# Performance work log

Hardware: AMD Instinct MI355X
Metric: run time of the kernel (lower is better)

## Reference

```python
import jax, jax.numpy as jnp
import numpy as np

# Module hyper-parameters (eval mode: remove_rand_on_eval=True => no random additional points)
B, H, C, E = 2, 8, 2048, 1024
D = 64          # head_size
KP = 8          # k (points per query per head)
P = 2 * KP      # num_points = k * 2**rank, rank = 1


def setup_inputs() -> dict:
    key = jax.random.key(0)
    ks = jax.random.split(key, 10)
    x = jax.random.normal(ks[0], (B, C, E), jnp.float32)
    attention_mask = jnp.ones((B, C), jnp.int32)  # accepted but unused, as in the torch forward
    # hyper() outputs (abstract in the class): continuous means in [0, C-1), positive sigmas, values
    means = jax.random.uniform(ks[1], (B, H, C, KP, 1), jnp.float32) * (C - 1)
    sigmas = jax.random.uniform(ks[2], (B, H, C, KP), jnp.float32) * 2.0 + 0.5
    values = jax.random.normal(ks[3], (B, H, C, KP), jnp.float32)
    s_in = 1.0 / np.sqrt(E).astype(np.float32)
    s_u = 1.0 / np.sqrt(H * D).astype(np.float32)
    Wk = jax.random.normal(ks[4], (E, H * D), jnp.float32) * s_in
    Wq = jax.random.normal(ks[5], (E, H * D), jnp.float32) * s_in
    Wv = jax.random.normal(ks[6], (E, H * D), jnp.float32) * s_in
    Wu = jax.random.normal(ks[7], (H * D, E), jnp.float32) * s_u
    bu = jnp.zeros((E,), jnp.float32)
    return dict(x=x, attention_mask=attention_mask, means=means, sigmas=sigmas,
                values=values, Wk=Wk, Wq=Wq, Wv=Wv, Wu=Wu, bu=bu)


def reference(x, attention_mask, means, sigmas, values, Wk, Wq, Wv, Wu, bu):
    b, c, e = x.shape
    h, d, kp, p = H, D, KP, P

    # ---- ngenerate (eval: only the 2**rank = 2 integer corners per mean, clamped in-range) ----
    m = means[..., 0]                                  # (b,h,c,k)
    i0 = jnp.clip(jnp.floor(m).astype(jnp.int32), 0, c - 1)
    i1 = jnp.clip(i0 + 1, 0, c - 1)
    idx = jnp.stack([i0, i1], axis=-1).reshape(b, h, c, p)   # (b,h,c,P)
    idx_fl = idx.astype(jnp.float32)

    # ---- densities: unnormalized Gaussian of each integer point under each of the k means ----
    diff = idx_fl[..., :, None] - m[..., None, :]            # (b,h,c,P,k)
    dens = jnp.exp(-0.5 * (diff / sigmas[..., None, :]) ** 2)

    # ---- nduplicates: zero densities of repeated index tuples (keep first occurrence) ----
    eq = idx[..., :, None] == idx[..., None, :]              # (b,h,c,P,P)
    earlier = jnp.tril(jnp.ones((p, p), bool), k=-1)         # q < p
    dup = jnp.any(eq & earlier, axis=-1)                     # (b,h,c,P)
    dens = jnp.where(dup[..., None], 0.0, dens)

    # normalize over dim=2 (context), exactly as the torch code does
    dens = dens / (dens.sum(axis=2, keepdims=True) + 1e-8)

    # density-weighted continuous values -> per-point weights
    weights = (values[..., None, :] * dens).sum(axis=-1)     # (b,h,c,P)

    # ---- projections ----
    inv_sqrt_d = 1.0 / np.sqrt(d).astype(np.float32)
    Kt = (x @ Wk).reshape(b, c, h, d).transpose(0, 2, 1, 3) * inv_sqrt_d  # (b,h,c,d)
    Qt = (x @ Wq).reshape(b, c, h, d).transpose(0, 2, 1, 3) * inv_sqrt_d
    Vt = (x @ Wv).reshape(b, c, h, d).transpose(0, 2, 1, 3)

    # ---- gather K/V at the sparse indices ----
    flat = idx.reshape(b, h, c * p, 1)
    Kg = jnp.take_along_axis(Kt, flat, axis=2).reshape(b, h, c, p, d)
    Vg = jnp.take_along_axis(Vt, flat, axis=2).reshape(b, h, c, p, d)

    dots = jnp.einsum('bhcd,bhcpd->bhcp', Qt, Kg)
    new_weights = jax.nn.softmax(weights * dots, axis=-1)    # (b,h,c,P)

    head_reps = jnp.einsum('bhcpd,bhcp->bhcd', Vg, new_weights)
    united = head_reps.transpose(0, 2, 1, 3).reshape(b, c, h * d)
    new_out = united @ Wu + bu

    # ---- scatter-add sparse weights into dense attention matrix ----
    bi = jnp.arange(b)[:, None, None, None]
    hi = jnp.arange(h)[None, :, None, None]
    ci = jnp.arange(c)[None, None, :, None]
    attentions = jnp.zeros((b, h, c, c), jnp.float32).at[bi, hi, ci, idx].add(new_weights)

    return new_out, attentions
```

## Files before the change

kernel.cpp:

```cpp
#include <hip/hip_runtime.h>
#include <math.h>
#include <stdint.h>

#define B_ 2
#define H_ 8
#define C_ 2048
#define E_ 1024
#define D_ 64
#define KP_ 8
#define P_ 16
#define HD_ 512
#define ROWS_ 32768
#define M_ 4096

typedef __bf16 bf16x8 __attribute__((ext_vector_type(8)));
typedef float f32x4 __attribute__((ext_vector_type(4)));
typedef uint16_t u16x8 __attribute__((ext_vector_type(8)));

__device__ inline uint16_t f2bf(float f) {
    union { float f; uint32_t u; } v; v.f = f;
    uint32_t u = v.u + 0x7FFF + ((v.u >> 16) & 1);
    return (uint16_t)(u >> 16);
}
__device__ inline float bf2f(uint16_t h) {
    union { uint32_t u; float f; } v; v.u = ((uint32_t)h) << 16;
    return v.f;
}

__device__ inline void gload16(const uint16_t* g, uint16_t* l) {
    __builtin_amdgcn_global_load_lds(
        (const __attribute__((address_space(1))) void*)g,
        (__attribute__((address_space(3))) void*)l, 16, 0, 0);
}

__global__ __launch_bounds__(256) void convert_x_kernel(
    const float* __restrict__ in, uint16_t* __restrict__ out)
{
    const int i = (blockIdx.x * 256 + threadIdx.x) * 8;
    const float4 a = *(const float4*)(in + i);
    const float4 b = *(const float4*)(in + i + 4);
    u16x8 o;
    o[0] = f2bf(a.x); o[1] = f2bf(a.y); o[2] = f2bf(a.z); o[3] = f2bf(a.w);
    o[4] = f2bf(b.x); o[5] = f2bf(b.y); o[6] = f2bf(b.z); o[7] = f2bf(b.w);
    *(u16x8*)(out + i) = o;
}

__global__ __launch_bounds__(256) void convert_wt_kernel(
    const float* __restrict__ Wq, const float* __restrict__ Wk,
    const float* __restrict__ Wv, const float* __restrict__ Wu,
    uint16_t* __restrict__ Wall, uint16_t* __restrict__ Wut)
{
    const int z = blockIdx.z;
    const float* in; uint16_t* out; int R, Cc; float scale;
    if (z == 0)      { in = Wq; out = Wall;                 R = E_;  Cc = HD_; scale = 0.125f; }
    else if (z == 1) { in = Wk; out = Wall + 512 * 1024;    R = E_;  Cc = HD_; scale = 0.125f; }
    else if (z == 2) { in = Wv; out = Wall + 1024 * 1024;   R = E_;  Cc = HD_; scale = 1.0f; }
    else             { in = Wu; out = Wut;                  R = HD_; Cc = E_;  scale = 1.0f; }
    const int tiles_x = Cc >> 5;
    const int tx = blockIdx.x % tiles_x;
    const int ty = blockIdx.x / tiles_x;
    const int r0 = ty * 32, c0 = tx * 32;
    __shared__ float t[32][33];
    const int lx = threadIdx.x & 31, ly = threadIdx.x >> 5;
#pragma unroll
    for (int i = 0; i < 4; ++i)
        t[ly * 4 + i][lx] = in[(size_t)(r0 + ly * 4 + i) * Cc + c0 + lx];
    __syncthreads();
#pragma unroll
    for (int i = 0; i < 4; ++i)
        out[(size_t)(c0 + ly * 4 + i) * R + r0 + lx] = f2bf(t[lx][ly * 4 + i] * scale);
}

__global__ __launch_bounds__(256) void gemm_qkv_kernel(
    const uint16_t* __restrict__ xb, const uint16_t* __restrict__ Wall,
    uint16_t* __restrict__ Qt, uint16_t* __restrict__ Kt,
    uint16_t* __restrict__ Vt)
{
    const int K = E_;
    const int m0 = blockIdx.y * 128;
    const int n0 = blockIdx.x * 128;
    const int z = n0 >> 9;
    uint16_t* __restrict__ Out = (z == 0) ? Qt : (z == 1) ? Kt : Vt;

    __shared__ __align__(16) uint16_t As[128 * 32];
    __shared__ __align__(16) uint16_t Bs[128 * 32];

    const int tid = threadIdx.x;
    const int w = tid >> 6, lane = tid & 63;
    const int wm = w & 1, wn = w >> 1;

    f32x4 acc[4][4] = {};

    const int r0s = (w * 2 + 0) * 16 + (lane >> 2);
    const int r1s = (w * 2 + 1) * 16 + (lane >> 2);
    const int ko  = (lane & 3) * 8;
    const uint16_t* gA0 = xb + (size_t)(m0 + r0s) * K + ko;
    const uint16_t* gA1 = xb + (size_t)(m0 + r1s) * K + ko;
    const uint16_t* gB0 = Wall + (size_t)(n0 + r0s) * K + ko;
    const uint16_t* gB1 = Wall + (size_t)(n0 + r1s) * K + ko;
    uint16_t* lA0 = &As[(w * 2 + 0) * 512];
    uint16_t* lA1 = &As[(w * 2 + 1) * 512];
    uint16_t* lB0 = &Bs[(w * 2 + 0) * 512];
    uint16_t* lB1 = &Bs[(w * 2 + 1) * 512];

    const int fr = lane & 15;
    const int fk = (lane >> 4) * 8;

    for (int k0 = 0; k0 < K; k0 += 32) {
        __syncthreads();
        gload16(gA0 + k0, lA0);
        gload16(gA1 + k0, lA1);
        gload16(gB0 + k0, lB0);
        gload16(gB1 + k0, lB1);
        __syncthreads();
        bf16x8 af[4], bf[4];
#pragma unroll
        for (int t = 0; t < 4; ++t) {
            af[t] = *(const bf16x8*)&As[(wm * 64 + t * 16 + fr) * 32 + fk];
            bf[t] = *(const bf16x8*)&Bs[(wn * 64 + t * 16 + fr) * 32 + fk];
        }
#pragma unroll
        for (int mt = 0; mt < 4; ++mt)
#pragma unroll
            for (int nt = 0; nt < 4; ++nt)
                acc[mt][nt] = __builtin_amdgcn_mfma_f32_16x16x32_bf16(
                    af[mt], bf[nt], acc[mt][nt], 0, 0, 0);
    }

#pragma unroll
    for (int mt = 0; mt < 4; ++mt) {
#pragma unroll
        for (int nt = 0; nt < 4; ++nt) {
            const int nl = (n0 & 511) + wn * 64 + nt * 16 + fr;
            const int h = nl >> 6, d = nl & 63;
#pragma unroll
            for (int r = 0; r < 4; ++r) {
                const int m = m0 + wm * 64 + mt * 16 + (lane >> 4) * 4 + r;
                const int b = m >> 11, c = m & (C_ - 1);
                Out[(((size_t)(b * H_ + h) * C_ + c) << 6) + d] =
                    f2bf(acc[mt][nt][r]);
            }
        }
    }
}

__global__ __launch_bounds__(256) void gemm_out_kernel(
    const uint16_t* __restrict__ U, const uint16_t* __restrict__ Wut,
    const float* __restrict__ bu, float* __restrict__ out)
{
    const int K = HD_;
    const int m0 = blockIdx.y * 128;
    const int n0 = blockIdx.x * 128;

    __shared__ __align__(16) uint16_t As[128 * 32];
    __shared__ __align__(16) uint16_t Bs[128 * 32];

    const int tid = threadIdx.x;
    const int w = tid >> 6, lane = tid & 63;
    const int wm = w & 1, wn = w >> 1;

    f32x4 acc[4][4] = {};

    const int r0s = (w * 2 + 0) * 16 + (lane >> 2);
    const int r1s = (w * 2 + 1) * 16 + (lane >> 2);
    const int ko  = (lane & 3) * 8;
    const uint16_t* gA0 = U + (size_t)(m0 + r0s) * K + ko;
    const uint16_t* gA1 = U + (size_t)(m0 + r1s) * K + ko;
    const uint16_t* gB0 = Wut + (size_t)(n0 + r0s) * K + ko;
    const uint16_t* gB1 = Wut + (size_t)(n0 + r1s) * K + ko;
    uint16_t* lA0 = &As[(w * 2 + 0) * 512];
    uint16_t* lA1 = &As[(w * 2 + 1) * 512];
    uint16_t* lB0 = &Bs[(w * 2 + 0) * 512];
    uint16_t* lB1 = &Bs[(w * 2 + 1) * 512];

    const int fr = lane & 15;
    const int fk = (lane >> 4) * 8;

    for (int k0 = 0; k0 < K; k0 += 32) {
        __syncthreads();
        gload16(gA0 + k0, lA0);
        gload16(gA1 + k0, lA1);
        gload16(gB0 + k0, lB0);
        gload16(gB1 + k0, lB1);
        __syncthreads();
        bf16x8 af[4], bf[4];
#pragma unroll
        for (int t = 0; t < 4; ++t) {
            af[t] = *(const bf16x8*)&As[(wm * 64 + t * 16 + fr) * 32 + fk];
            bf[t] = *(const bf16x8*)&Bs[(wn * 64 + t * 16 + fr) * 32 + fk];
        }
#pragma unroll
        for (int mt = 0; mt < 4; ++mt)
#pragma unroll
            for (int nt = 0; nt < 4; ++nt)
                acc[mt][nt] = __builtin_amdgcn_mfma_f32_16x16x32_bf16(
                    af[mt], bf[nt], acc[mt][nt], 0, 0, 0);
    }

#pragma unroll
    for (int mt = 0; mt < 4; ++mt) {
#pragma unroll
        for (int nt = 0; nt < 4; ++nt) {
            const int n = n0 + wn * 64 + nt * 16 + fr;
            const float bias = bu[n];
#pragma unroll
            for (int r = 0; r < 4; ++r) {
                const int m = m0 + wm * 64 + mt * 16 + (lane >> 4) * 4 + r;
                out[(size_t)m * E_ + n] = acc[mt][nt][r] + bias;
            }
        }
    }
}

__global__ __launch_bounds__(256) void dens_sum_kernel(
    const float* __restrict__ means, const float* __restrict__ sigmas,
    float* __restrict__ S)
{
    const int row = blockIdx.x * 256 + threadIdx.x;
    const int lane = threadIdx.x & 63;
    const int bh = row >> 11;

    const float* mrow = means + (size_t)row * 8;
    const float* srow = sigmas + (size_t)row * 8;
    const float4 ma = *(const float4*)(mrow);
    const float4 mb = *(const float4*)(mrow + 4);
    const float4 sa = *(const float4*)(srow);
    const float4 sb = *(const float4*)(srow + 4);
    const float mm[8] = {ma.x, ma.y, ma.z, ma.w, mb.x, mb.y, mb.z, mb.w};
    const float sg[8] = {sa.x, sa.y, sa.z, sa.w, sb.x, sb.y, sb.z, sb.w};

    int idx[16];
#pragma unroll
    for (int j = 0; j < 8; ++j) {
        int i0 = (int)floorf(mm[j]);
        i0 = min(max(i0, 0), C_ - 1);
        idx[2 * j] = i0;
        idx[2 * j + 1] = min(i0 + 1, C_ - 1);
    }
    unsigned dupm = 0;
#pragma unroll
    for (int p = 1; p < 16; ++p) {
        bool d = false;
#pragma unroll
        for (int q = 0; q < 15; ++q)
            if (q < p) d = d || (idx[q] == idx[p]);
        if (d) dupm |= (1u << p);
    }

#pragma unroll
    for (int p = 0; p < 16; ++p) {
        const float fi = (float)idx[p];
        const bool dup = (dupm >> p) & 1u;
#pragma unroll
        for (int kk = 0; kk < 8; ++kk) {
            const float t = (fi - mm[kk]) / sg[kk];
            float val = dup ? 0.0f : expf(-0.5f * t * t);
#pragma unroll
            for (int off = 1; off < 64; off <<= 1)
                val += __shfl_xor(val, off);
            if (lane == 0)
                atomicAdd(&S[bh * 128 + p * 8 + kk], val);
        }
    }
}

__global__ __launch_bounds__(256) void attn_kernel(
    const float* __restrict__ means, const float* __restrict__ sigmas,
    const float* __restrict__ values, const float* __restrict__ S,
    const uint16_t* __restrict__ Qt, const uint16_t* __restrict__ Kt,
    const uint16_t* __restrict__ Vt, uint16_t* __restrict__ united,
    float* __restrict__ attn)
{
    __shared__ float rowbuf[4][2048];
    const int w = threadIdx.x >> 6;
    const int lane = threadIdx.x & 63;
    const int row = blockIdx.x * 4 + w;
    const int bh = row >> 11;
    const int c = row & (C_ - 1);
    const int b = bh >> 3;
    const int h = bh & 7;

    const float* mrow = means + (size_t)row * 8;
    const float4 ma = *(const float4*)(mrow);
    const float4 mb = *(const float4*)(mrow + 4);
    const float mm[8] = {ma.x, ma.y, ma.z, ma.w, mb.x, mb.y, mb.z, mb.w};

    int idx[16];
#pragma unroll
    for (int j = 0; j < 8; ++j) {
        int i0 = (int)floorf(mm[j]);
        i0 = min(max(i0, 0), C_ - 1);
        idx[2 * j] = i0;
        idx[2 * j + 1] = min(i0 + 1, C_ - 1);
    }

    const int lp = lane & 15;
    int myidx = 0;
#pragma unroll
    for (int q = 0; q < 16; ++q)
        if (q == lp) myidx = idx[q];
    float wp = 0.0f;
    if (lane < 16) {
        bool dup = false;
#pragma unroll
        for (int q = 0; q < 15; ++q)
            dup = dup || ((q < lane) && (idx[q] == myidx));
        if (!dup) {
            const float* srow = sigmas + (size_t)row * 8;
            const float* vrow = values + (size_t)row * 8;
            const float4 sa = *(const float4*)(srow);
            const float4 sb = *(const float4*)(srow + 4);
            const float4 va = *(const float4*)(vrow);
            const float4 vb = *(const float4*)(vrow + 4);
            const float sg[8] = {sa.x, sa.y, sa.z, sa.w, sb.x, sb.y, sb.z, sb.w};
            const float vl[8] = {va.x, va.y, va.z, va.w, vb.x, vb.y, vb.z, vb.w};
            const float* Sp = S + bh * 128 + lane * 8;
            const float4 Sa = *(const float4*)(Sp);
            const float4 Sb = *(const float4*)(Sp + 4);
            const float Sv[8] = {Sa.x, Sa.y, Sa.z, Sa.w, Sb.x, Sb.y, Sb.z, Sb.w};
            const float fi = (float)myidx;
#pragma unroll
            for (int kk = 0; kk < 8; ++kk) {
                const float t = (fi - mm[kk]) / sg[kk];
                const float e = expf(-0.5f * t * t);
                wp = fmaf(vl[kk], e / (Sv[kk] + 1e-8f), wp);
            }
        }
    }

    const int p = lane >> 2, g = lane & 3;
    int kidx = 0;
#pragma unroll
    for (int q = 0; q < 16; ++q)
        if (q == p) kidx = idx[q];

    const uint16_t* Qrow = Qt + ((size_t)row << 6);
    const uint16_t* Krow = Kt + ((((size_t)bh << 11) + kidx) << 6);
    const u16x8 qa = *(const u16x8*)(Qrow + g * 16);
    const u16x8 qb = *(const u16x8*)(Qrow + g * 16 + 8);
    const u16x8 ka = *(const u16x8*)(Krow + g * 16);
    const u16x8 kb = *(const u16x8*)(Krow + g * 16 + 8);
    float dot = 0.0f;
#pragma unroll
    for (int j = 0; j < 8; ++j) {
        dot = fmaf(bf2f(qa[j]), bf2f(ka[j]), dot);
        dot = fmaf(bf2f(qb[j]), bf2f(kb[j]), dot);
    }
    dot += __shfl_xor(dot, 1);
    dot += __shfl_xor(dot, 2);

    const float wvp = __shfl(wp, p);
    const float logit = wvp * dot;

    float mx = logit;
#pragma unroll
    for (int off = 4; off < 64; off <<= 1)
        mx = fmaxf(mx, __shfl_xor(mx, off));
    const float e = expf(logit - mx);
    float se = e;
#pragma unroll
    for (int off = 4; off < 64; off <<= 1)
        se += __shfl_xor(se, off);
    const float sm = e / se;

    float smv[16];
#pragma unroll
    for (int q = 0; q < 16; ++q)
        smv[q] = __shfl(sm, q * 4);
    const float myw = __shfl(sm, lp * 4);

    const uint16_t* Vbh = Vt + ((size_t)bh << 17);
    float acc = 0.0f;
#pragma unroll
    for (int q = 0; q < 16; ++q)
        acc = fmaf(bf2f(Vbh[((size_t)idx[q] << 6) + lane]), smv[q], acc);
    united[((size_t)(b * C_ + c)) * HD_ + h * 64 + lane] = f2bf(acc);

    const f32x4 z4 = {0.f, 0.f, 0.f, 0.f};
#pragma unroll
    for (int j = 0; j < 8; ++j)
        *(f32x4*)&rowbuf[w][(j * 64 + lane) * 4] = z4;
    __syncthreads();
    if (lane < 16) atomicAdd(&rowbuf[w][myidx], myw);
    __syncthreads();
    float* arow = attn + ((size_t)row << 11);
#pragma unroll
    for (int j = 0; j < 8; ++j) {
        const int o = (j * 64 + lane) * 4;
        __builtin_nontemporal_store(*(const f32x4*)&rowbuf[w][o], (f32x4*)&arow[o]);
    }
}

extern "C" void kernel_launch(void* const* d_in, const int* in_sizes, int n_in,
                              void* d_out, int out_size, void* d_ws,
                              size_t ws_size, hipStream_t stream) {
    const float* x      = (const float*)d_in[0];
    const float* means  = (const float*)d_in[2];
    const float* sigmas = (const float*)d_in[3];
    const float* values = (const float*)d_in[4];
    const float* Wk     = (const float*)d_in[5];
    const float* Wq     = (const float*)d_in[6];
    const float* Wv     = (const float*)d_in[7];
    const float* Wu     = (const float*)d_in[8];
    const float* bu     = (const float*)d_in[9];

    float* out  = (float*)d_out;
    float* attn = out + (size_t)M_ * E_;

    uint16_t* wsp = (uint16_t*)d_ws;
    uint16_t* xb     = wsp;
    uint16_t* Wall   = xb + 4194304;
    uint16_t* Wut    = Wall + 1572864;
    uint16_t* Qt     = Wut + 524288;
    uint16_t* Kt     = Qt + 2097152;
    uint16_t* Vt     = Kt + 2097152;
    uint16_t* united = Vt + 2097152;
    float*    S      = (float*)(united + 2097152);

    (void)hipMemsetAsync(S, 0, 2048 * sizeof(float), stream);

    convert_x_kernel<<<2048, 256, 0, stream>>>(x, xb);
    convert_wt_kernel<<<dim3(512, 1, 4), 256, 0, stream>>>(
        Wq, Wk, Wv, Wu, Wall, Wut);
    dens_sum_kernel<<<128, 256, 0, stream>>>(means, sigmas, S);
    gemm_qkv_kernel<<<dim3(12, 32), 256, 0, stream>>>(xb, Wall, Qt, Kt, Vt);
    attn_kernel<<<ROWS_ / 4, 256, 0, stream>>>(
        means, sigmas, values, S, Qt, Kt, Vt, united, attn);
    gemm_out_kernel<<<dim3(8, 32), 256, 0, stream>>>(united, Wut, bu, out);
}
```

Measured before the change: 423.4 us.

## Fuse prep kernels into one launch and stage QKV epilogue through LDS

Merges the x conversion, weight transpose/convert and density-sum kernels into a single prep kernel dispatched by block index, cutting two kernel launches. The QKV GEMM epilogue now writes accumulators to an enlarged shared tile and then stores 16-byte vectors to the head-major outputs instead of scattered 2-byte stores. The larger shared allocation (about 34 KB) may lower occupancy for the GEMM, and the fused kernel's shared tile is allocated for every block type.

```diff
diff --git a/kernel.cpp b/kernel.cpp
--- a/kernel.cpp
+++ b/kernel.cpp
@@ -33,42 +33,95 @@
         (__attribute__((address_space(3))) void*)l, 16, 0, 0);
 }
 
-__global__ __launch_bounds__(256) void convert_x_kernel(
-    const float* __restrict__ in, uint16_t* __restrict__ out)
-{
-    const int i = (blockIdx.x * 256 + threadIdx.x) * 8;
-    const float4 a = *(const float4*)(in + i);
-    const float4 b = *(const float4*)(in + i + 4);
-    u16x8 o;
-    o[0] = f2bf(a.x); o[1] = f2bf(a.y); o[2] = f2bf(a.z); o[3] = f2bf(a.w);
-    o[4] = f2bf(b.x); o[5] = f2bf(b.y); o[6] = f2bf(b.z); o[7] = f2bf(b.w);
-    *(u16x8*)(out + i) = o;
-}
-
-__global__ __launch_bounds__(256) void convert_wt_kernel(
+__global__ __launch_bounds__(256) void prep_kernel(
+    const float* __restrict__ x,
     const float* __restrict__ Wq, const float* __restrict__ Wk,
     const float* __restrict__ Wv, const float* __restrict__ Wu,
-    uint16_t* __restrict__ Wall, uint16_t* __restrict__ Wut)
+    const float* __restrict__ means, const float* __restrict__ sigmas,
+    uint16_t* __restrict__ xb, uint16_t* __restrict__ Wall,
+    uint16_t* __restrict__ Wut, float* __restrict__ S)
 {
-    const int z = blockIdx.z;
-    const float* in; uint16_t* out; int R, Cc; float scale;
-    if (z == 0)      { in = Wq; out = Wall;                 R = E_;  Cc = HD_; scale = 0.125f; }
-    else if (z == 1) { in = Wk; out = Wall + 512 * 1024;    R = E_;  Cc = HD_; scale = 0.125f; }
-    else if (z == 2) { in = Wv; out = Wall + 1024 * 1024;   R = E_;  Cc = HD_; scale = 1.0f; }
-    else             { in = Wu; out = Wut;                  R = HD_; Cc = E_;  scale = 1.0f; }
-    const int tiles_x = Cc >> 5;
-    const int tx = blockIdx.x % tiles_x;
-    const int ty = blockIdx.x / tiles_x;
-    const int r0 = ty * 32, c0 = tx * 32;
-    __shared__ float t[32][33];
-    const int lx = threadIdx.x & 31, ly = threadIdx.x >> 5;
-#pragma unroll
-    for (int i = 0; i < 4; ++i)
-        t[ly * 4 + i][lx] = in[(size_t)(r0 + ly * 4 + i) * Cc + c0 + lx];
-    __syncthreads();
-#pragma unroll
-    for (int i = 0; i < 4; ++i)
-        out[(size_t)(c0 + ly * 4 + i) * R + r0 + lx] = f2bf(t[lx][ly * 4 + i] * scale);
+    const int bx = blockIdx.x;
+    if (bx < 2048) {
+        const int i = (bx * 256 + threadIdx.x) * 8;
+        const float4 a = *(const float4*)(x + i);
+        const float4 b = *(const float4*)(x + i + 4);
+        u16x8 o;
+        o[0] = f2bf(a.x); o[1] = f2bf(a.y); o[2] = f2bf(a.z); o[3] = f2bf(a.w);
+        o[4] = f2bf(b.x); o[5] = f2bf(b.y); o[6] = f2bf(b.z); o[7] = f2bf(b.w);
+        *(u16x8*)(xb + i) = o;
+        return;
+    }
+    if (bx < 4096) {
+        const int t = bx - 2048;
+        const int z = t >> 9;
+        const float* in; uint16_t* out; int R, Cc; float scale;
+        if (z == 0)      { in = Wq; out = Wall;               R = E_;  Cc = HD_; scale = 0.125f; }
+        else if (z == 1) { in = Wk; out = Wall + 512 * 1024;  R = E_;  Cc = HD_; scale = 0.125f; }
+        else if (z == 2) { in = Wv; out = Wall + 1024 * 1024; R = E_;  Cc = HD_; scale = 1.0f; }
+        else             { in = Wu; out = Wut;                R = HD_; Cc = E_;  scale = 1.0f; }
+        const int tiles_x = Cc >> 5;
+        const int ti = t & 511;
+        const int tx = ti % tiles_x;
+        const int ty = ti / tiles_x;
+        const int r0 = ty * 32, c0 = tx * 32;
+        __shared__ float tbuf[32][33];
+        const int lx = threadIdx.x & 31, ly = threadIdx.x >> 5;
+#pragma unroll
+        for (int i = 0; i < 4; ++i)
+            tbuf[ly * 4 + i][lx] = in[(size_t)(r0 + ly * 4 + i) * Cc + c0 + lx];
+        __syncthreads();
+#pragma unroll
+        for (int i = 0; i < 4; ++i)
+            out[(size_t)(c0 + ly * 4 + i) * R + r0 + lx] =
+                f2bf(tbuf[lx][ly * 4 + i] * scale);
+        return;
+    }
+    const int row = (bx - 4096) * 256 + threadIdx.x;
+    const int lane = threadIdx.x & 63;
+    const int bh = row >> 11;
+
+    const float* mrow = means + (size_t)row * 8;
+    const float* srow = sigmas + (size_t)row * 8;
+    const float4 ma = *(const float4*)(mrow);
+    const float4 mb = *(const float4*)(mrow + 4);
+    const float4 sa = *(const float4*)(srow);
+    const float4 sb = *(const float4*)(srow + 4);
+    const float mm[8] = {ma.x, ma.y, ma.z, ma.w, mb.x, mb.y, mb.z, mb.w};
+    const float sg[8] = {sa.x, sa.y, sa.z, sa.w, sb.x, sb.y, sb.z, sb.w};
+
+    int idx[16];
+#pragma unroll
+    for (int j = 0; j < 8; ++j) {
+        int i0 = (int)floorf(mm[j]);
+        i0 = min(max(i0, 0), C_ - 1);
+        idx[2 * j] = i0;
+        idx[2 * j + 1] = min(i0 + 1, C_ - 1);
+    }
+    unsigned dupm = 0;
+#pragma unroll
+    for (int p = 1; p < 16; ++p) {
+        bool d = false;
+#pragma unroll
+        for (int q = 0; q < 15; ++q)
+            if (q < p) d = d || (idx[q] == idx[p]);
+        if (d) dupm |= (1u << p);
+    }
+#pragma unroll
+    for (int p = 0; p < 16; ++p) {
+        const float fi = (float)idx[p];
+        const bool dup = (dupm >> p) & 1u;
+#pragma unroll
+        for (int kk = 0; kk < 8; ++kk) {
+            const float t = (fi - mm[kk]) / sg[kk];
+            float val = dup ? 0.0f : expf(-0.5f * t * t);
+#pragma unroll
+            for (int off = 1; off < 64; off <<= 1)
+                val += __shfl_xor(val, off);
+            if (lane == 0)
+                atomicAdd(&S[bh * 128 + p * 8 + kk], val);
+        }
+    }
 }
 
 __global__ __launch_bounds__(256) void gemm_qkv_kernel(
@@ -82,8 +135,9 @@
     const int z = n0 >> 9;
     uint16_t* __restrict__ Out = (z == 0) ? Qt : (z == 1) ? Kt : Vt;
 
-    __shared__ __align__(16) uint16_t As[128 * 32];
-    __shared__ __align__(16) uint16_t Bs[128 * 32];
+    __shared__ __align__(16) uint16_t smem[128 * 136];
+    uint16_t* As = smem;
+    uint16_t* Bs = smem + 4096;
 
     const int tid = threadIdx.x;
     const int w = tid >> 6, lane = tid & 63;
@@ -127,20 +181,29 @@
                     af[mt], bf[nt], acc[mt][nt], 0, 0, 0);
     }
 
-#pragma unroll
-    for (int mt = 0; mt < 4; ++mt) {
+    __syncthreads();
+#pragma unroll
+    for (int mt = 0; mt < 4; ++mt)
 #pragma unroll
         for (int nt = 0; nt < 4; ++nt) {
-            const int nl = (n0 & 511) + wn * 64 + nt * 16 + fr;
-            const int h = nl >> 6, d = nl & 63;
+            const int col = wn * 64 + nt * 16 + fr;
 #pragma unroll
             for (int r = 0; r < 4; ++r) {
-                const int m = m0 + wm * 64 + mt * 16 + (lane >> 4) * 4 + r;
-                const int b = m >> 11, c = m & (C_ - 1);
-                Out[(((size_t)(b * H_ + h) * C_ + c) << 6) + d] =
-                    f2bf(acc[mt][nt][r]);
+                const int rw = wm * 64 + mt * 16 + (lane >> 4) * 4 + r;
+                smem[rw * 136 + col] = f2bf(acc[mt][nt][r]);
             }
         }
+    __syncthreads();
+#pragma unroll
+    for (int it = 0; it < 8; ++it) {
+        const int e0 = (it * 256 + tid) * 8;
+        const int row = e0 >> 7, tcol = e0 & 127;
+        const int nl = (n0 & 511) + tcol;
+        const int h = nl >> 6, d = nl & 63;
+        const int m = m0 + row;
+        const int b = m >> 11, c = m & (C_ - 1);
+        *(u16x8*)&Out[(((size_t)(b * H_ + h) * C_ + c) << 6) + d] =
+            *(const u16x8*)&smem[row * 136 + tcol];
     }
 }
 
@@ -208,58 +271,6 @@
                 const int m = m0 + wm * 64 + mt * 16 + (lane >> 4) * 4 + r;
                 out[(size_t)m * E_ + n] = acc[mt][nt][r] + bias;
             }
-        }
-    }
-}
-
-__global__ __launch_bounds__(256) void dens_sum_kernel(
-    const float* __restrict__ means, const float* __restrict__ sigmas,
-    float* __restrict__ S)
-{
-    const int row = blockIdx.x * 256 + threadIdx.x;
-    const int lane = threadIdx.x & 63;
-    const int bh = row >> 11;
-
-    const float* mrow = means + (size_t)row * 8;
-    const float* srow = sigmas + (size_t)row * 8;
-    const float4 ma = *(const float4*)(mrow);
-    const float4 mb = *(const float4*)(mrow + 4);
-    const float4 sa = *(const float4*)(srow);
-    const float4 sb = *(const float4*)(srow + 4);
-    const float mm[8] = {ma.x, ma.y, ma.z, ma.w, mb.x, mb.y, mb.z, mb.w};
-    const float sg[8] = {sa.x, sa.y, sa.z, sa.w, sb.x, sb.y, sb.z, sb.w};
-
-    int idx[16];
-#pragma unroll
-    for (int j = 0; j < 8; ++j) {
-        int i0 = (int)floorf(mm[j]);
-        i0 = min(max(i0, 0), C_ - 1);
-        idx[2 * j] = i0;
-        idx[2 * j + 1] = min(i0 + 1, C_ - 1);
-    }
-    unsigned dupm = 0;
-#pragma unroll
-    for (int p = 1; p < 16; ++p) {
-        bool d = false;
-#pragma unroll
-        for (int q = 0; q < 15; ++q)
-            if (q < p) d = d || (idx[q] == idx[p]);
-        if (d) dupm |= (1u << p);
-    }
-
-#pragma unroll
-    for (int p = 0; p < 16; ++p) {
-        const float fi = (float)idx[p];
-        const bool dup = (dupm >> p) & 1u;
-#pragma unroll
-        for (int kk = 0; kk < 8; ++kk) {
-            const float t = (fi - mm[kk]) / sg[kk];
-            float val = dup ? 0.0f : expf(-0.5f * t * t);
-#pragma unroll
-            for (int off = 1; off < 64; off <<= 1)
-                val += __shfl_xor(val, off);
-            if (lane == 0)
-                atomicAdd(&S[bh * 128 + p * 8 + kk], val);
         }
     }
 }
@@ -419,10 +430,8 @@
 
     (void)hipMemsetAsync(S, 0, 2048 * sizeof(float), stream);
 
-    convert_x_kernel<<<2048, 256, 0, stream>>>(x, xb);
-    convert_wt_kernel<<<dim3(512, 1, 4), 256, 0, stream>>>(
-        Wq, Wk, Wv, Wu, Wall, Wut);
-    dens_sum_kernel<<<128, 256, 0, stream>>>(means, sigmas, S);
+    prep_kernel<<<4224, 256, 0, stream>>>(
+        x, Wq, Wk, Wv, Wu, means, sigmas, xb, Wall, Wut, S);
     gemm_qkv_kernel<<<dim3(12, 32), 256, 0, stream>>>(xb, Wall, Qt, Kt, Vt);
     attn_kernel<<<ROWS_ / 4, 256, 0, stream>>>(
         means, sigmas, values, S, Qt, Kt, Vt, united, attn);
```

Measured after the change: 417.0 us. No clear change (-1.5%).
